# Kernel optimization log

Measured on AMD Instinct MI355X. Metric: run time of the kernel, lower is better.

The kernel has to match this reference:

```python
import jax, jax.numpy as jnp
import numpy as np
from jax import lax

B, CIN, COUT, WDIM, K, H, W_ = 8, 512, 512, 512, 3, 64, 64

def setup_inputs() -> dict:
    key = jax.random.key(0)
    ks = jax.random.split(key, 7)
    x = jax.random.normal(ks[0], (B, CIN, H, W_), dtype=jnp.float32)
    w = jax.random.normal(ks[1], (B, WDIM), dtype=jnp.float32)
    noise = jax.random.normal(ks[2], (B, COUT, H, W_), dtype=jnp.float32)
    # params (kaiming-ish scale for weight; demodulation normalizes anyway)
    weight = jax.random.normal(ks[3], (1, COUT, CIN, K, K), dtype=jnp.float32) * 0.05
    affine_w = jax.random.normal(ks[4], (CIN, WDIM), dtype=jnp.float32) * (1.0 / np.sqrt(WDIM))
    affine_b = jnp.zeros((CIN,), dtype=jnp.float32)
    bias = jnp.zeros((COUT,), dtype=jnp.float32)
    return {"x": x, "w": w, "noise": noise, "weight": weight,
            "affine_w": affine_w, "affine_b": affine_b, "bias": bias}

def reference(x, w, noise, weight, affine_w, affine_b, bias):
    b, cin, h, ww = x.shape
    cout, k = weight.shape[1], weight.shape[3]
    # style: affine(w) + 1
    s = jnp.einsum('bd,cd->bc', w, affine_w) + affine_b          # [B, Cin]
    s = s[:, None, :, None, None] + 1.0                           # [B,1,Cin,1,1]
    w_mod = weight * s                                            # [B,Cout,Cin,k,k]
    d = lax.rsqrt(jnp.sum(w_mod * w_mod, axis=(2, 3, 4), keepdims=True) + 1e-8)
    w_mod = w_mod * d
    # grouped conv: groups = B
    x_ = x.reshape(1, b * cin, h, ww)
    w_ = w_mod.reshape(b * cout, cin, k, k)
    pad = k // 2
    y = lax.conv_general_dilated(
        x_, w_, window_strides=(1, 1), padding=[(pad, pad), (pad, pad)],
        feature_group_count=b,
        dimension_numbers=('NCHW', 'OIHW', 'NCHW'))
    y = y.reshape(b, cout, h, ww)
    y = y + noise + bias[None, :, None, None]
    return jnp.where(y >= 0, y, 0.2 * y)
```

## Files before the change

kernel.cpp:

```cpp
#include <hip/hip_runtime.h>
#include <hip/hip_bf16.h>


#define CIN   512
#define COUT  512
#define KDIM  4608
#define HWPIX 4096

typedef __attribute__((ext_vector_type(8))) __bf16 bf16x8;
typedef __attribute__((ext_vector_type(4))) float  f32x4;

__device__ __forceinline__ unsigned short f2bf(float f){
  union { float f; unsigned int u; } v; v.f = f;
  unsigned int u = v.u;
  u += 0x7fffu + ((u >> 16) & 1u);
  return (unsigned short)(u >> 16);
}

#define GLDS16(g, l) __builtin_amdgcn_global_load_lds(                      \
    (const __attribute__((address_space(1))) unsigned int*)(g),             \
    (__attribute__((address_space(3))) unsigned int*)(l), 16, 0, 0)

__global__ void style_k(const float* __restrict__ w, const float* __restrict__ aw,
                        const float* __restrict__ ab, float* __restrict__ styles){
  int wid = threadIdx.x >> 6, lane = threadIdx.x & 63;
  int gid = blockIdx.x * 4 + wid;
  int b = gid >> 9, c = gid & 511;
  const float* wb = w + b * 512;
  const float* ar = aw + c * 512;
  float sum = 0.f;
  for (int j = lane; j < 512; j += 64) sum += wb[j] * ar[j];
  for (int off = 32; off; off >>= 1) sum += __shfl_down(sum, off, 64);
  if (lane == 0) styles[gid] = sum + ab[c] + 1.0f;
}

__global__ void modw_k(const float* __restrict__ weight, const float* __restrict__ styles,
                       unsigned short* __restrict__ wmod){
  int o = blockIdx.x;
  int t = threadIdx.x;
  const float* wrow = weight + (size_t)o * KDIM;
  float wv[18];
#pragma unroll
  for (int it = 0; it < 18; ++it) wv[it] = wrow[it * 256 + t];
  __shared__ unsigned short sw[9 * 520];
  __shared__ float red[4];
  int wid = t >> 6, lane = t & 63;
  for (int b = 0; b < 8; ++b){
    const float* st = styles + b * 512;
    float vals[18];
    float part = 0.f;
#pragma unroll
    for (int it = 0; it < 18; ++it){
      int idx = it * 256 + t;
      int i = idx / 9;
      float v = wv[it] * st[i];
      vals[it] = v;
      part += v * v;
    }
    for (int off = 32; off; off >>= 1) part += __shfl_down(part, off, 64);
    if (lane == 0) red[wid] = part;
    __syncthreads();
    float d = rsqrtf(red[0] + red[1] + red[2] + red[3] + 1e-8f);
#pragma unroll
    for (int it = 0; it < 18; ++it){
      int idx = it * 256 + t;
      int i = idx / 9;
      int tap = idx - i * 9;
      sw[tap * 520 + i] = f2bf(vals[it] * d);
    }
    __syncthreads();
    unsigned int* orow32 = (unsigned int*)(wmod + ((size_t)(b * 512 + o)) * KDIM);
#pragma unroll
    for (int it = 0; it < 9; ++it){
      int u = it * 256 + t;
      int e = u * 2;
      int tap2 = e >> 9, i2 = e & 511;
      orow32[u] = *(const unsigned int*)&sw[tap2 * 520 + i2];
    }
    __syncthreads();
  }
}

__global__ void xpose_k(const float* __restrict__ x, unsigned short* __restrict__ xpad){
  int h = blockIdx.x, cg = blockIdx.y, b = blockIdx.z;
  int c0 = cg * 64;
  __shared__ unsigned short lds[64][66];
  int t = threadIdx.x;
  const float* xb = x + (((size_t)(b * 512 + c0)) * 64 + h) * 64;
#pragma unroll
  for (int it = 0; it < 16; ++it){
    int idx = it * 256 + t;
    int cl = idx >> 6, wl = idx & 63;
    lds[wl][cl] = f2bf(xb[(size_t)cl * 4096 + wl]);
  }
  if (t < 64){
    int which = t >> 5;
    int ch2 = (t & 31) * 2;
    int wl = which ? 65 : 0;
    *(unsigned int*)&xpad[(((size_t)b * 66 + h + 1) * 66 + wl) * 512 + c0 + ch2] = 0u;
  }
  if (h == 0 || h == 63){
    int row = (h == 0) ? 0 : 65;
    for (int u = t; u < 66 * 32; u += 256){
      int wl = u >> 5, ch2 = (u & 31) * 2;
      *(unsigned int*)&xpad[(((size_t)b * 66 + row) * 66 + wl) * 512 + c0 + ch2] = 0u;
    }
  }
  __syncthreads();
#pragma unroll
  for (int it = 0; it < 2; ++it){
    int idx = it * 256 + t;
    int wl = idx >> 3, ch = idx & 7;
    unsigned int u0 = *(const unsigned int*)&lds[wl][ch * 8 + 0];
    unsigned int u1 = *(const unsigned int*)&lds[wl][ch * 8 + 2];
    unsigned int u2 = *(const unsigned int*)&lds[wl][ch * 8 + 4];
    unsigned int u3 = *(const unsigned int*)&lds[wl][ch * 8 + 6];
    int off = ((b * 66 + h + 1) * 66 + (wl + 1)) * 512 + c0 + ch * 8;
    *(uint4*)&xpad[off] = make_uint4(u0, u1, u2, u3);
  }
}

__global__ __launch_bounds__(256, 2) void conv_gemm(
    const unsigned short* __restrict__ wmod, const unsigned short* __restrict__ xpad,
    const float* __restrict__ noise, const float* __restrict__ bias,
    float* __restrict__ out){
  __shared__ unsigned short As[2][256 * 32];
  __shared__ unsigned short Bs[2][128 * 32];
  int g = blockIdx.x;
  int xcd = g & 7, sl = g >> 3;
  int b = xcd, mt = sl >> 5, nt = sl & 31;
  int m0 = mt * 256, n0 = nt * 128;
  int h0 = nt * 2;
  int tid = threadIdx.x, wid = tid >> 6, lane = tid & 63;
  int wm = wid >> 1, wn = wid & 1;
  int lr = lane >> 2;
  int lc = lane & 3;
  int sc = lc ^ ((lr >> 1) & 3);

  const unsigned short* wbase = wmod + ((size_t)(b * 512 + m0)) * KDIM;
  int aoffG[4];
#pragma unroll
  for (int i = 0; i < 4; ++i)
    aoffG[i] = ((wid * 64 + i * 16 + lr)) * KDIM + sc * 8;

  const unsigned short* xb = xpad + (size_t)b * 66 * 66 * 512;
  int boffG[2];
#pragma unroll
  for (int i = 0; i < 2; ++i){
    int p = wid * 32 + i * 16 + lr;
    boffG[i] = ((h0 + (p >> 6) + 1) * 66 + ((p & 63) + 1)) * 512 + sc * 8;
  }
  int albase[4], blbase[2];
#pragma unroll
  for (int i = 0; i < 4; ++i) albase[i] = (wid * 64 + i * 16) * 32;
#pragma unroll
  for (int i = 0; i < 2; ++i) blbase[i] = (wid * 32 + i * 16) * 32;

  int fm = lane & 15;
  int cidx = lane >> 4;
  int rk = cidx ^ ((fm >> 1) & 3);
  int apo[8], bpo[4];
#pragma unroll
  for (int i = 0; i < 8; ++i) apo[i] = (wm * 128 + i * 16 + fm) * 32 + rk * 8;
#pragma unroll
  for (int j = 0; j < 4; ++j) bpo[j] = (wn * 64 + j * 16 + fm) * 32 + rk * 8;

  f32x4 acc[8][4];
#pragma unroll
  for (int i = 0; i < 8; ++i)
#pragma unroll
    for (int j = 0; j < 4; ++j) acc[i][j] = (f32x4){0.f, 0.f, 0.f, 0.f};

  for (int ks = 0; ks < 72; ++ks){
    int tap = ks >> 3;
    int c0  = (ks & 7) << 6;
    int k0  = (tap << 9) + c0;
    int dy3 = tap / 3;
    int bshift = (((dy3 - 1) * 66 + (tap - dy3 * 3 - 1)) << 9) + c0;
    __syncthreads();
#pragma unroll
    for (int i = 0; i < 4; ++i){
      GLDS16(wbase + aoffG[i] + k0,      &As[0][albase[i]]);
      GLDS16(wbase + aoffG[i] + k0 + 32, &As[1][albase[i]]);
    }
#pragma unroll
    for (int i = 0; i < 2; ++i){
      GLDS16(xb + boffG[i] + bshift,      &Bs[0][blbase[i]]);
      GLDS16(xb + boffG[i] + bshift + 32, &Bs[1][blbase[i]]);
    }
    __syncthreads();
#pragma unroll
    for (int s = 0; s < 2; ++s){
      bf16x8 af[8], bfr[4];
#pragma unroll
      for (int i = 0; i < 8; ++i) af[i]  = *(const bf16x8*)&As[s][apo[i]];
#pragma unroll
      for (int j = 0; j < 4; ++j) bfr[j] = *(const bf16x8*)&Bs[s][bpo[j]];
#pragma unroll
      for (int i = 0; i < 8; ++i)
#pragma unroll
        for (int j = 0; j < 4; ++j)
          acc[i][j] = __builtin_amdgcn_mfma_f32_16x16x32_bf16(af[i], bfr[j], acc[i][j], 0, 0, 0);
    }
  }

  int quad = lane >> 4;
#pragma unroll
  for (int i = 0; i < 8; ++i){
    int o_base = m0 + wm * 128 + i * 16 + quad * 4;
#pragma unroll
    for (int j = 0; j < 4; ++j){
      int n = n0 + wn * 64 + j * 16 + fm;
#pragma unroll
      for (int r = 0; r < 4; ++r){
        int o = o_base + r;
        size_t idx = ((size_t)(b * 512 + o)) * HWPIX + n;
        float v = acc[i][j][r] + noise[idx] + bias[o];
        out[idx] = (v >= 0.f) ? v : 0.2f * v;
      }
    }
  }
}

extern "C" void kernel_launch(void* const* d_in, const int* in_sizes, int n_in,
                              void* d_out, int out_size, void* d_ws, size_t ws_size,
                              hipStream_t stream) {
  const float* x        = (const float*)d_in[0];
  const float* w        = (const float*)d_in[1];
  const float* noise    = (const float*)d_in[2];
  const float* weight   = (const float*)d_in[3];
  const float* affine_w = (const float*)d_in[4];
  const float* affine_b = (const float*)d_in[5];
  const float* bias     = (const float*)d_in[6];
  float* out = (float*)d_out;

  float* styles = (float*)d_ws;
  unsigned short* wmod = (unsigned short*)((char*)d_ws + 16384);
  unsigned short* xpad = (unsigned short*)((char*)d_ws + 16384 + 37748736ull);

  style_k<<<dim3(1024), 256, 0, stream>>>(w, affine_w, affine_b, styles);
  modw_k <<<dim3(512), 256, 0, stream>>>(weight, styles, wmod);
  xpose_k<<<dim3(64, 8, 8), 256, 0, stream>>>(x, xpad);
  conv_gemm<<<dim3(512), 256, 0, stream>>>(wmod, xpad, noise, bias, out);
}
```

Measured before the change: 338.4 us.

## Rewrite conv GEMM as 256x256 tile, 8-wave, 4-stage pipelined schedule; parallelize modw over batch

The conv GEMM moves from 256x128 tiles with 4 waves and a 2-buffer load/sync/compute loop to 256x256 tiles with 8 waves. It uses a 4-slot LDS ring of 64-wide K chunks and splits each K step into four MFMA quadrants. Global-to-LDS loads are interleaved between quadrants with partial vmcnt waits and raw barriers, and MFMA runs at raised priority, so that load latency is hidden and per-tile reuse increases. The grid halves to 256 blocks, which lowers parallelism and raises LDS use to 128KB per block. modw_k now launches one block per (o,b) instead of looping over b, to get more parallelism in weight modulation.

```diff
diff --git a/kernel.cpp b/kernel.cpp
--- a/kernel.cpp
+++ b/kernel.cpp
@@ -37,47 +37,42 @@
 __global__ void modw_k(const float* __restrict__ weight, const float* __restrict__ styles,
                        unsigned short* __restrict__ wmod){
   int o = blockIdx.x;
+  int b = blockIdx.y;
   int t = threadIdx.x;
   const float* wrow = weight + (size_t)o * KDIM;
-  float wv[18];
-#pragma unroll
-  for (int it = 0; it < 18; ++it) wv[it] = wrow[it * 256 + t];
+  const float* st = styles + b * 512;
   __shared__ unsigned short sw[9 * 520];
   __shared__ float red[4];
   int wid = t >> 6, lane = t & 63;
-  for (int b = 0; b < 8; ++b){
-    const float* st = styles + b * 512;
-    float vals[18];
-    float part = 0.f;
-#pragma unroll
-    for (int it = 0; it < 18; ++it){
-      int idx = it * 256 + t;
-      int i = idx / 9;
-      float v = wv[it] * st[i];
-      vals[it] = v;
-      part += v * v;
-    }
-    for (int off = 32; off; off >>= 1) part += __shfl_down(part, off, 64);
-    if (lane == 0) red[wid] = part;
-    __syncthreads();
-    float d = rsqrtf(red[0] + red[1] + red[2] + red[3] + 1e-8f);
-#pragma unroll
-    for (int it = 0; it < 18; ++it){
-      int idx = it * 256 + t;
-      int i = idx / 9;
-      int tap = idx - i * 9;
-      sw[tap * 520 + i] = f2bf(vals[it] * d);
-    }
-    __syncthreads();
-    unsigned int* orow32 = (unsigned int*)(wmod + ((size_t)(b * 512 + o)) * KDIM);
-#pragma unroll
-    for (int it = 0; it < 9; ++it){
-      int u = it * 256 + t;
-      int e = u * 2;
-      int tap2 = e >> 9, i2 = e & 511;
-      orow32[u] = *(const unsigned int*)&sw[tap2 * 520 + i2];
-    }
-    __syncthreads();
+  float vals[18];
+  float part = 0.f;
+#pragma unroll
+  for (int it = 0; it < 18; ++it){
+    int idx = it * 256 + t;
+    int i = idx / 9;
+    float v = wrow[idx] * st[i];
+    vals[it] = v;
+    part += v * v;
+  }
+  for (int off = 32; off; off >>= 1) part += __shfl_down(part, off, 64);
+  if (lane == 0) red[wid] = part;
+  __syncthreads();
+  float d = rsqrtf(red[0] + red[1] + red[2] + red[3] + 1e-8f);
+#pragma unroll
+  for (int it = 0; it < 18; ++it){
+    int idx = it * 256 + t;
+    int i = idx / 9;
+    int tap = idx - i * 9;
+    sw[tap * 520 + i] = f2bf(vals[it] * d);
+  }
+  __syncthreads();
+  unsigned int* orow32 = (unsigned int*)(wmod + ((size_t)(b * 512 + o)) * KDIM);
+#pragma unroll
+  for (int it = 0; it < 9; ++it){
+    int u = it * 256 + t;
+    int e = u * 2;
+    int tap2 = e >> 9, i2 = e & 511;
+    orow32[u] = *(const unsigned int*)&sw[tap2 * 520 + i2];
   }
 }
 
@@ -120,106 +115,176 @@
   }
 }
 
-__global__ __launch_bounds__(256, 2) void conv_gemm(
+__device__ __forceinline__ int bshift_of(int t){
+  int tap = t >> 3;
+  int dy = (tap * 11) >> 5;
+  int dx = tap - dy * 3;
+  return (((dy - 1) * 66 + (dx - 1)) << 9) + ((t & 7) << 6);
+}
+
+__global__ __launch_bounds__(512, 2) void conv_gemm(
     const unsigned short* __restrict__ wmod, const unsigned short* __restrict__ xpad,
     const float* __restrict__ noise, const float* __restrict__ bias,
     float* __restrict__ out){
-  __shared__ unsigned short As[2][256 * 32];
-  __shared__ unsigned short Bs[2][128 * 32];
+  __shared__ unsigned short As[4][128 * 64];
+  __shared__ unsigned short Bs[4][128 * 64];
   int g = blockIdx.x;
-  int xcd = g & 7, sl = g >> 3;
-  int b = xcd, mt = sl >> 5, nt = sl & 31;
-  int m0 = mt * 256, n0 = nt * 128;
-  int h0 = nt * 2;
-  int tid = threadIdx.x, wid = tid >> 6, lane = tid & 63;
-  int wm = wid >> 1, wn = wid & 1;
-  int lr = lane >> 2;
-  int lc = lane & 3;
-  int sc = lc ^ ((lr >> 1) & 3);
+  int b = g & 7, sl = g >> 3;
+  int mt = sl >> 4, nt = sl & 15;
+  int m0 = mt * 256, n0 = nt * 256, h0 = nt * 4;
+  int tid = threadIdx.x, lane = tid & 63, wid = tid >> 6;
+  int wmp = wid >> 2, wnp = wid & 3;
+  int lf = lane & 15, lg = lane >> 4;
 
   const unsigned short* wbase = wmod + ((size_t)(b * 512 + m0)) * KDIM;
-  int aoffG[4];
-#pragma unroll
-  for (int i = 0; i < 4; ++i)
-    aoffG[i] = ((wid * 64 + i * 16 + lr)) * KDIM + sc * 8;
-
-  const unsigned short* xb = xpad + (size_t)b * 66 * 66 * 512;
-  int boffG[2];
-#pragma unroll
-  for (int i = 0; i < 2; ++i){
-    int p = wid * 32 + i * 16 + lr;
-    boffG[i] = ((h0 + (p >> 6) + 1) * 66 + ((p & 63) + 1)) * 512 + sc * 8;
-  }
-  int albase[4], blbase[2];
-#pragma unroll
-  for (int i = 0; i < 4; ++i) albase[i] = (wid * 64 + i * 16) * 32;
-#pragma unroll
-  for (int i = 0; i < 2; ++i) blbase[i] = (wid * 32 + i * 16) * 32;
-
-  int fm = lane & 15;
-  int cidx = lane >> 4;
-  int rk = cidx ^ ((fm >> 1) & 3);
-  int apo[8], bpo[4];
-#pragma unroll
-  for (int i = 0; i < 8; ++i) apo[i] = (wm * 128 + i * 16 + fm) * 32 + rk * 8;
-#pragma unroll
-  for (int j = 0; j < 4; ++j) bpo[j] = (wn * 64 + j * 16 + fm) * 32 + rk * 8;
-
-  f32x4 acc[8][4];
-#pragma unroll
-  for (int i = 0; i < 8; ++i)
-#pragma unroll
-    for (int j = 0; j < 4; ++j) acc[i][j] = (f32x4){0.f, 0.f, 0.f, 0.f};
-
-  for (int ks = 0; ks < 72; ++ks){
-    int tap = ks >> 3;
-    int c0  = (ks & 7) << 6;
-    int k0  = (tap << 9) + c0;
-    int dy3 = tap / 3;
-    int bshift = (((dy3 - 1) * 66 + (tap - dy3 * 3 - 1)) << 9) + c0;
-    __syncthreads();
-#pragma unroll
-    for (int i = 0; i < 4; ++i){
-      GLDS16(wbase + aoffG[i] + k0,      &As[0][albase[i]]);
-      GLDS16(wbase + aoffG[i] + k0 + 32, &As[1][albase[i]]);
-    }
-#pragma unroll
-    for (int i = 0; i < 2; ++i){
-      GLDS16(xb + boffG[i] + bshift,      &Bs[0][blbase[i]]);
-      GLDS16(xb + boffG[i] + bshift + 32, &Bs[1][blbase[i]]);
-    }
-    __syncthreads();
-#pragma unroll
-    for (int s = 0; s < 2; ++s){
-      bf16x8 af[8], bfr[4];
-#pragma unroll
-      for (int i = 0; i < 8; ++i) af[i]  = *(const bf16x8*)&As[s][apo[i]];
-#pragma unroll
-      for (int j = 0; j < 4; ++j) bfr[j] = *(const bf16x8*)&Bs[s][bpo[j]];
-#pragma unroll
-      for (int i = 0; i < 8; ++i)
-#pragma unroll
-        for (int j = 0; j < 4; ++j)
-          acc[i][j] = __builtin_amdgcn_mfma_f32_16x16x32_bf16(af[i], bfr[j], acc[i][j], 0, 0, 0);
-    }
-  }
-
-  int quad = lane >> 4;
-#pragma unroll
-  for (int i = 0; i < 8; ++i){
-    int o_base = m0 + wm * 128 + i * 16 + quad * 4;
-#pragma unroll
-    for (int j = 0; j < 4; ++j){
-      int n = n0 + wn * 64 + j * 16 + fm;
-#pragma unroll
-      for (int r = 0; r < 4; ++r){
-        int o = o_base + r;
-        size_t idx = ((size_t)(b * 512 + o)) * HWPIX + n;
-        float v = acc[i][j][r] + noise[idx] + bias[o];
-        out[idx] = (v >= 0.f) ? v : 0.2f * v;
-      }
-    }
-  }
+  const unsigned short* xb    = xpad + (size_t)b * (66 * 66 * 512);
+
+  int srow  = tid >> 3;
+  int sc    = (tid & 7) ^ (srow & 7);
+  int aoffg  = srow * KDIM + sc * 8;
+  int boffg0 = ((h0 + 1) * 66 + srow + 1) * 512 + sc * 8;
+  int boffg1 = ((h0 + 2) * 66 + srow + 1) * 512 + sc * 8;
+
+  int arow[4], brow[2];
+#pragma unroll
+  for (int i = 0; i < 4; ++i) arow[i] = (wmp * 64 + i * 16 + lf) * 64;
+#pragma unroll
+  for (int j = 0; j < 2; ++j) brow[j] = (wnp * 32 + j * 16 + lf) * 64;
+  int pch0 = ((lg    ) ^ (lane & 7)) * 8;
+  int pch1 = ((lg + 4) ^ (lane & 7)) * 8;
+
+  f32x4 acc[2][2][4][2];
+#pragma unroll
+  for (int a0 = 0; a0 < 2; ++a0)
+#pragma unroll
+    for (int a1 = 0; a1 < 2; ++a1)
+#pragma unroll
+      for (int a2 = 0; a2 < 4; ++a2)
+#pragma unroll
+        for (int a3 = 0; a3 < 2; ++a3) acc[a0][a1][a2][a3] = (f32x4){0.f, 0.f, 0.f, 0.f};
+
+  bf16x8 af[4][2], bq0[2][2], bq1[2][2];
+
+#define STAGE_A(t_, h_, s_) do {                                              \
+    const unsigned short* gpa_ = wbase + (size_t)(h_) * (128 * KDIM) + (t_) * 64; \
+    GLDS16(gpa_ + aoffg,             &As[s_][tid * 8]);                       \
+    GLDS16(gpa_ + aoffg + 64 * KDIM, &As[s_][(512 + tid) * 8]);               \
+  } while (0)
+
+#define STAGE_B(t_, h_, s_) do {                                              \
+    const unsigned short* gpb_ = xb + (h_) * (2 * 66 * 512) + bshift_of(t_);  \
+    GLDS16(gpb_ + boffg0, &Bs[s_][tid * 8]);                                  \
+    GLDS16(gpb_ + boffg1, &Bs[s_][(512 + tid) * 8]);                          \
+  } while (0)
+
+#define LOAD_A(s_) do {                                                       \
+    _Pragma("unroll") for (int fi_ = 0; fi_ < 4; ++fi_){                      \
+      af[fi_][0] = *(const bf16x8*)&As[s_][arow[fi_] + pch0];                 \
+      af[fi_][1] = *(const bf16x8*)&As[s_][arow[fi_] + pch1]; }               \
+  } while (0)
+
+#define LOAD_B(s_, B_) do {                                                   \
+    _Pragma("unroll") for (int fj_ = 0; fj_ < 2; ++fj_){                      \
+      B_[fj_][0] = *(const bf16x8*)&Bs[s_][brow[fj_] + pch0];                 \
+      B_[fj_][1] = *(const bf16x8*)&Bs[s_][brow[fj_] + pch1]; }               \
+  } while (0)
+
+#define MFMA_Q(MH_, NH_, B_) do {                                             \
+    __builtin_amdgcn_s_setprio(1);                                            \
+    _Pragma("unroll") for (int fi_ = 0; fi_ < 4; ++fi_)                       \
+    _Pragma("unroll") for (int fj_ = 0; fj_ < 2; ++fj_){                      \
+      acc[MH_][NH_][fi_][fj_] = __builtin_amdgcn_mfma_f32_16x16x32_bf16(      \
+          af[fi_][0], B_[fj_][0], acc[MH_][NH_][fi_][fj_], 0, 0, 0);          \
+      acc[MH_][NH_][fi_][fj_] = __builtin_amdgcn_mfma_f32_16x16x32_bf16(      \
+          af[fi_][1], B_[fj_][1], acc[MH_][NH_][fi_][fj_], 0, 0, 0); }        \
+    __builtin_amdgcn_s_setprio(0);                                            \
+  } while (0)
+
+#define SYNC_MID() do { __builtin_amdgcn_s_barrier();                         \
+    asm volatile("s_waitcnt lgkmcnt(0)"); } while (0)
+#define SYNC_END() __builtin_amdgcn_s_barrier()
+#define VMW6() asm volatile("s_waitcnt vmcnt(6)" ::: "memory")
+#define VMW0() asm volatile("s_waitcnt vmcnt(0)" ::: "memory")
+
+  STAGE_A(0, 0, 0); STAGE_B(0, 0, 0); STAGE_B(0, 1, 1); STAGE_A(0, 1, 1);
+  STAGE_A(1, 0, 2); STAGE_B(1, 0, 2); STAGE_B(1, 1, 3);
+  VMW6();
+  __builtin_amdgcn_s_barrier();
+
+#pragma unroll 1
+  for (int it = 0; it < 35; ++it){
+    int T = it * 2;
+    LOAD_A(0); LOAD_B(0, bq0);
+    STAGE_A(T + 1, 1, 3);
+    SYNC_MID(); MFMA_Q(0, 0, bq0); SYNC_END();
+    LOAD_B(1, bq1);
+    STAGE_A(T + 2, 0, 0);
+    SYNC_MID(); MFMA_Q(0, 1, bq1); SYNC_END();
+    LOAD_A(1);
+    STAGE_B(T + 2, 0, 0);
+    SYNC_MID(); MFMA_Q(1, 0, bq0); SYNC_END();
+    STAGE_B(T + 2, 1, 1);
+    VMW6();
+    SYNC_MID(); MFMA_Q(1, 1, bq1); SYNC_END();
+    LOAD_A(2); LOAD_B(2, bq0);
+    STAGE_A(T + 2, 1, 1);
+    SYNC_MID(); MFMA_Q(0, 0, bq0); SYNC_END();
+    LOAD_B(3, bq1);
+    STAGE_A(T + 3, 0, 2);
+    SYNC_MID(); MFMA_Q(0, 1, bq1); SYNC_END();
+    LOAD_A(3);
+    STAGE_B(T + 3, 0, 2);
+    SYNC_MID(); MFMA_Q(1, 0, bq0); SYNC_END();
+    STAGE_B(T + 3, 1, 3);
+    VMW6();
+    SYNC_MID(); MFMA_Q(1, 1, bq1); SYNC_END();
+  }
+
+  LOAD_A(0); LOAD_B(0, bq0);
+  STAGE_A(71, 1, 3);
+  SYNC_MID(); MFMA_Q(0, 0, bq0); SYNC_END();
+  LOAD_B(1, bq1);
+  SYNC_MID(); MFMA_Q(0, 1, bq1); SYNC_END();
+  LOAD_A(1);
+  SYNC_MID(); MFMA_Q(1, 0, bq0); SYNC_END();
+  VMW0();
+  SYNC_MID(); MFMA_Q(1, 1, bq1); SYNC_END();
+  LOAD_A(2); LOAD_B(2, bq0);
+  SYNC_MID(); MFMA_Q(0, 0, bq0); SYNC_END();
+  LOAD_B(3, bq1);
+  SYNC_MID(); MFMA_Q(0, 1, bq1); SYNC_END();
+  LOAD_A(3);
+  SYNC_MID(); MFMA_Q(1, 0, bq0); SYNC_END();
+  SYNC_MID(); MFMA_Q(1, 1, bq1);
+
+#undef STAGE_A
+#undef STAGE_B
+#undef LOAD_A
+#undef LOAD_B
+#undef MFMA_Q
+#undef SYNC_MID
+#undef SYNC_END
+#undef VMW6
+#undef VMW0
+
+#pragma unroll
+  for (int MH = 0; MH < 2; ++MH)
+#pragma unroll
+    for (int NH = 0; NH < 2; ++NH)
+#pragma unroll
+      for (int fi = 0; fi < 4; ++fi)
+#pragma unroll
+        for (int fj = 0; fj < 2; ++fj){
+          int o_base = m0 + MH * 128 + wmp * 64 + fi * 16 + lg * 4;
+          int n = n0 + NH * 128 + wnp * 32 + fj * 16 + lf;
+#pragma unroll
+          for (int r = 0; r < 4; ++r){
+            int o = o_base + r;
+            size_t idx = ((size_t)(b * 512 + o)) * HWPIX + n;
+            float v = acc[MH][NH][fi][fj][r] + noise[idx] + bias[o];
+            out[idx] = (v >= 0.f) ? v : 0.2f * v;
+          }
+        }
 }
 
 extern "C" void kernel_launch(void* const* d_in, const int* in_sizes, int n_in,
@@ -239,7 +304,7 @@
   unsigned short* xpad = (unsigned short*)((char*)d_ws + 16384 + 37748736ull);
 
   style_k<<<dim3(1024), 256, 0, stream>>>(w, affine_w, affine_b, styles);
-  modw_k <<<dim3(512), 256, 0, stream>>>(weight, styles, wmod);
+  modw_k <<<dim3(512, 8), 256, 0, stream>>>(weight, styles, wmod);
   xpose_k<<<dim3(64, 8, 8), 256, 0, stream>>>(x, xpad);
-  conv_gemm<<<dim3(512), 256, 0, stream>>>(wmod, xpad, noise, bias, out);
-}
+  conv_gemm<<<dim3(256), 512, 0, stream>>>(wmod, xpad, noise, bias, out);
+}
```

New measurement: 324.5 us. -4.1%, faster.
